# Optimization experiments

Hardware: AMD Instinct MI355X
Metric: run time of the kernel (lower is better)

## Reference

```python
import jax, jax.numpy as jnp
import numpy as np

P, M, DG, F, H, DH = 2000, 150, 2000, 256, 4, 64
N1, N2 = P + M, P + DG          # adj1 nodes (patient+med), adj2 nodes (patient+diag)
E1, E2, EGP, EGM = 137600, 256000, 64000, 4800
GNN_LAYERS = 2
SA_HID = 128


def setup_inputs() -> dict:
    key = jax.random.key(0)
    ks = jax.random.split(key, 32)
    ri = lambda k, n, hi: jax.random.randint(k, (n,), 0, hi, dtype=jnp.int32)
    rn = lambda k, shape, scale: (jax.random.normal(k, shape, dtype=jnp.float32) * scale)
    inp = {
        'adj1_rows': ri(ks[0], E1, N1), 'adj1_cols': ri(ks[1], E1, N1),
        'adj1_vals': jax.random.uniform(ks[2], (E1,), dtype=jnp.float32),
        'adj2_rows': ri(ks[3], E2, N2), 'adj2_cols': ri(ks[4], E2, N2),
        'adj2_vals': jax.random.uniform(ks[5], (E2,), dtype=jnp.float32),
        'g0_src': ri(ks[6], EGP, P), 'g0_dst': ri(ks[7], EGP, P),
        'g1_src': ri(ks[8], EGP, P), 'g1_dst': ri(ks[9], EGP, P),
        'g2_src': ri(ks[10], EGM, M), 'g2_dst': ri(ks[11], EGM, M),
        'g3_src': ri(ks[12], EGM, M), 'g3_dst': ri(ks[13], EGM, M),
        'keepRate': 1,
        # learned parameters (xavier-ish scales)
        'pEmbed': rn(ks[14], (P, F), 0.05),
        'mEmbed': rn(ks[15], (M, F), 0.05),
        'dEmbed': rn(ks[16], (DG, F), 0.05),
        'gat_W': rn(ks[17], (4, F, H * DH), (2.0 / (F + H * DH)) ** 0.5),
        'gat_al': rn(ks[18], (4, H, DH), 0.1),
        'gat_ar': rn(ks[19], (4, H, DH), 0.1),
        'gat_b': jnp.zeros((4, H * DH), dtype=jnp.float32),
        'sa_W1': rn(ks[20], (H * DH, SA_HID), (2.0 / (H * DH + SA_HID)) ** 0.5),
        'sa_b1': jnp.zeros((SA_HID,), dtype=jnp.float32),
        'sa_W2': rn(ks[21], (SA_HID, 1), 0.1),
        'out_W': rn(ks[22], (2 * F, M), (2.0 / (2 * F + M)) ** 0.5),
        'out_b': jnp.zeros((M,), dtype=jnp.float32),
    }
    return inp


def _spmm(rows, cols, vals, x, n):
    # sparse adj @ x via gather + segment_sum
    return jax.ops.segment_sum(vals[:, None] * x[cols], rows, num_segments=n)


def _seg_softmax(e, seg, n):
    m = jax.ops.segment_max(e, seg, num_segments=n)          # [n, H]
    ex = jnp.exp(e - m[seg])
    s = jax.ops.segment_sum(ex, seg, num_segments=n)
    return ex / (s[seg] + 1e-9)


def _gat(h, W, al, ar, b, src, dst, n):
    # DGL GATConv, feat/attn dropout = 0, negative_slope = 0.2, activation = elu
    feat = (h @ W).reshape(n, H, DH)                          # [n, H, DH]
    el = (feat * al[None]).sum(-1)                            # [n, H]
    er = (feat * ar[None]).sum(-1)
    e = jax.nn.leaky_relu(el[src] + er[dst], negative_slope=0.2)  # [E, H]
    alpha = _seg_softmax(e, dst, n)                           # softmax over in-edges per dst
    out = jax.ops.segment_sum(alpha[:, :, None] * feat[src], dst, num_segments=n)
    out = out + b.reshape(1, H, DH)
    return jax.nn.elu(out).reshape(n, H * DH)


def _sem_att(z, W1, b1, W2):
    # z: [N, K, F]; shared projection; beta over K meta-paths
    w = (jnp.tanh(z @ W1 + b1) @ W2).mean(0)                  # [K, 1]
    beta = jax.nn.softmax(w, axis=0)                          # [K, 1]
    return (beta[None] * z).sum(1)                            # [N, F]


def reference(adj1_rows, adj1_cols, adj1_vals, adj2_rows, adj2_cols, adj2_vals,
              g0_src, g0_dst, g1_src, g1_dst, g2_src, g2_dst, g3_src, g3_dst,
              keepRate, pEmbed, mEmbed, dEmbed, gat_W, gat_al, gat_ar, gat_b,
              sa_W1, sa_b1, sa_W2, out_W, out_b):
    embeds1 = jnp.concatenate([pEmbed, mEmbed], axis=0)       # [N1, F]
    embeds2 = jnp.concatenate([pEmbed, dEmbed], axis=0)       # [N2, F]
    lat1, lat2 = embeds1, embeds2
    acc1 = jnp.zeros_like(embeds1)
    acc2 = jnp.zeros_like(embeds2)
    for _ in range(GNN_LAYERS):
        lat1 = jax.nn.leaky_relu(_spmm(adj1_rows, adj1_cols, adj1_vals, lat1, N1), negative_slope=0.5)
        lat2 = jax.nn.leaky_relu(_spmm(adj2_rows, adj2_cols, adj2_vals, lat2, N2), negative_slope=0.5)
        acc1 = acc1 + lat1
        acc2 = acc2 + lat2
    p1, m_gcn = acc1[:P], acc1[P:]
    p2, d_gcn = acc2[:P], acc2[P:]

    e0 = _gat(p1, gat_W[0], gat_al[0], gat_ar[0], gat_b[0], g0_src, g0_dst, P)
    e1 = _gat(p2, gat_W[1], gat_al[1], gat_ar[1], gat_b[1], g1_src, g1_dst, P)
    e2 = _gat(m_gcn, gat_W[2], gat_al[2], gat_ar[2], gat_b[2], g2_src, g2_dst, M)
    e3 = _gat(m_gcn, gat_W[3], gat_al[3], gat_ar[3], gat_b[3], g3_src, g3_dst, M)

    patient = _sem_att(jnp.stack([e0, e1], axis=1), sa_W1, sa_b1, sa_W2)  # [P, F]
    med = _sem_att(jnp.stack([e2, e3], axis=1), sa_W1, sa_b1, sa_W2)      # [M, F]

    # broadcasted pairwise concat -> ReLU -> Linear -> sum over pairing axis
    pm = jnp.concatenate([
        jnp.broadcast_to(patient[:, None, :], (P, M, F)),
        jnp.broadcast_to(med[None, :, :], (P, M, F)),
    ], axis=-1).reshape(P * M, 2 * F)
    simi = (jax.nn.relu(pm) @ out_W + out_b).reshape(P, M, M)
    simi_pm = simi.sum(axis=1)                                # [P, M]
    return (simi_pm, d_gcn, med, m_gcn, patient)
```

## Files before the change

### kernel.cpp

```cpp
#include <hip/hip_runtime.h>
#include <cmath>
#include <cstdint>

constexpr int P  = 2000, M = 150, DG = 2000, F = 256, H = 4, DH = 64;
constexpr int N1 = P + M;
constexpr int N2 = P + DG;
constexpr int E1 = 137600, E2 = 256000, EGP = 64000, EGM = 4800;
constexpr int SA_HID = 128;

constexpr int HO1 = E1, HO2 = E1 + E2, HO3 = HO2 + EGP, HO4 = HO3 + EGP,
              HO5 = HO4 + EGM, HOE = HO5 + EGM;

constexpr int CAP_A = 160;
constexpr int CAP_G = 96;
constexpr int OVF_CAP = 4096;

__global__ __launch_bounds__(256) void k_build(
    const int* __restrict__ a1r, const int* __restrict__ a1c, const float* __restrict__ a1v,
    const int* __restrict__ a2r, const int* __restrict__ a2c, const float* __restrict__ a2v,
    const int* __restrict__ d0, const int* __restrict__ s0,
    const int* __restrict__ d1, const int* __restrict__ s1,
    const int* __restrict__ d2, const int* __restrict__ s2,
    const int* __restrict__ d3, const int* __restrict__ s3,
    int* cur1, uint2* ell1, int* cur2, uint2* ell2,
    int* cu0, unsigned* eg0, int* cu1, unsigned* eg1,
    int* cu2, unsigned* eg2, int* cu3, unsigned* eg3,
    int* __restrict__ ovf_n, int4* __restrict__ ovf) {
  int tid = blockIdx.x * 256 + threadIdx.x;
  int T = gridDim.x * 256;
  auto edge = [&](int i) {
    if (i >= HOE) return;
    if (i < HO1) {
      int r = a1r[i];
      int slot = atomicAdd(&cur1[r], 1);
      uint2 pl = {(unsigned)a1c[i], __float_as_uint(a1v[i])};
      if (slot < CAP_A) ell1[(size_t)r * CAP_A + slot] = pl;
      else { int o = atomicAdd(&ovf_n[0], 1); if (o < OVF_CAP) ovf[0 * OVF_CAP + o] = make_int4(r, (int)pl.x, (int)pl.y, 0); }
    } else if (i < HO2) {
      int j = i - HO1;
      int r = a2r[j];
      int slot = atomicAdd(&cur2[r], 1);
      uint2 pl = {(unsigned)a2c[j], __float_as_uint(a2v[j])};
      if (slot < CAP_A) ell2[(size_t)r * CAP_A + slot] = pl;
      else { int o = atomicAdd(&ovf_n[1], 1); if (o < OVF_CAP) ovf[1 * OVF_CAP + o] = make_int4(r, (int)pl.x, (int)pl.y, 0); }
    } else if (i < HO3) {
      int j = i - HO2; int r = d0[j];
      int slot = atomicAdd(&cu0[r], 1);
      if (slot < CAP_G) eg0[(size_t)r * CAP_G + slot] = (unsigned)s0[j];
      else { int o = atomicAdd(&ovf_n[2], 1); if (o < OVF_CAP) ovf[2 * OVF_CAP + o] = make_int4(r, s0[j], 0, 0); }
    } else if (i < HO4) {
      int j = i - HO3; int r = d1[j];
      int slot = atomicAdd(&cu1[r], 1);
      if (slot < CAP_G) eg1[(size_t)r * CAP_G + slot] = (unsigned)s1[j];
      else { int o = atomicAdd(&ovf_n[3], 1); if (o < OVF_CAP) ovf[3 * OVF_CAP + o] = make_int4(r, s1[j], 0, 0); }
    } else if (i < HO5) {
      int j = i - HO4; int r = d2[j];
      int slot = atomicAdd(&cu2[r], 1);
      if (slot < CAP_G) eg2[(size_t)r * CAP_G + slot] = (unsigned)s2[j];
      else { int o = atomicAdd(&ovf_n[4], 1); if (o < OVF_CAP) ovf[4 * OVF_CAP + o] = make_int4(r, s2[j], 0, 0); }
    } else {
      int j = i - HO5; int r = d3[j];
      int slot = atomicAdd(&cu3[r], 1);
      if (slot < CAP_G) eg3[(size_t)r * CAP_G + slot] = (unsigned)s3[j];
      else { int o = atomicAdd(&ovf_n[5], 1); if (o < OVF_CAP) ovf[5 * OVF_CAP + o] = make_int4(r, s3[j], 0, 0); }
    }
  };
  edge(tid);
  edge(tid + T);
  edge(tid + 2 * T);
  edge(tid + 3 * T);
}

template<int LAYER>
__global__ __launch_bounds__(256) void k_spmm(
    const int* __restrict__ cur1, const uint2* __restrict__ ell1,
    const int* __restrict__ cur2, const uint2* __restrict__ ell2,
    const int* __restrict__ ovf_n, const int4* __restrict__ ovf,
    const float* __restrict__ pE, const float* __restrict__ mE, const float* __restrict__ dE,
    float* __restrict__ lat1, float* __restrict__ lat2,
    float* __restrict__ acc1, float* __restrict__ acc2,
    float* __restrict__ out_mgcn, float* __restrict__ out_dgcn) {
  int gw = (blockIdx.x * 256 + threadIdx.x) >> 6;
  if (gw >= N1 + N2) return;
  int lane = threadIdx.x & 63;
  bool g2 = gw >= N1;
  int row = g2 ? gw - N1 : gw;
  const uint2* pe = (g2 ? ell2 : ell1) + (size_t)row * CAP_A;
  const float* latin = g2 ? lat2 : lat1;
  const float* tailE = g2 ? dE : mE;
  int deg = (g2 ? cur2 : cur1)[row];
  int dn = deg < CAP_A ? deg : CAP_A;
  int fo = lane << 2;
  float4 s = {0.f, 0.f, 0.f, 0.f};
  auto fetch = [&](int c) -> float4 {
    const float* b;
    if (LAYER == 1) b = (c < P) ? (pE + (size_t)c * F) : (tailE + (size_t)(c - P) * F);
    else            b = latin + (size_t)c * F;
    return *(const float4*)(b + fo);
  };
  int i = 0;
  for (; i + 4 <= dn; i += 4) {
    uint2 m0 = pe[i], m1 = pe[i + 1], m2 = pe[i + 2], m3 = pe[i + 3];
    float v0 = __uint_as_float(m0.y), v1 = __uint_as_float(m1.y),
          v2 = __uint_as_float(m2.y), v3 = __uint_as_float(m3.y);
    float4 a0 = fetch((int)m0.x), a1 = fetch((int)m1.x),
           a2 = fetch((int)m2.x), a3 = fetch((int)m3.x);
    s.x += v0 * a0.x + v1 * a1.x + v2 * a2.x + v3 * a3.x;
    s.y += v0 * a0.y + v1 * a1.y + v2 * a2.y + v3 * a3.y;
    s.z += v0 * a0.z + v1 * a1.z + v2 * a2.z + v3 * a3.z;
    s.w += v0 * a0.w + v1 * a1.w + v2 * a2.w + v3 * a3.w;
  }
  for (; i < dn; ++i) {
    uint2 m = pe[i];
    float v = __uint_as_float(m.y);
    float4 a = fetch((int)m.x);
    s.x += v * a.x; s.y += v * a.y; s.z += v * a.z; s.w += v * a.w;
  }
  {
    int gi = g2 ? 1 : 0;
    int on = ovf_n[gi];
    if (on > 0) {
      const int4* ol = ovf + gi * OVF_CAP;
      for (int k = 0; k < on; ++k) {
        int4 e = ol[k];
        if (e.x == row) {
          float v = __int_as_float(e.z);
          float4 a = fetch(e.y);
          s.x += v * a.x; s.y += v * a.y; s.z += v * a.z; s.w += v * a.w;
        }
      }
    }
  }
  float4 l;
  l.x = s.x > 0.f ? s.x : 0.5f * s.x;
  l.y = s.y > 0.f ? s.y : 0.5f * s.y;
  l.z = s.z > 0.f ? s.z : 0.5f * s.z;
  l.w = s.w > 0.f ? s.w : 0.5f * s.w;
  if (LAYER == 1) {
    *(float4*)((g2 ? lat2 : lat1) + (size_t)row * F + fo) = l;
  } else {
    float4 b = *(const float4*)(latin + (size_t)row * F + fo);
    float4 a = {b.x + l.x, b.y + l.y, b.z + l.z, b.w + l.w};
    *(float4*)((g2 ? acc2 : acc1) + (size_t)row * F + fo) = a;
    if (row >= P)
      *(float4*)((g2 ? out_dgcn : out_mgcn) + (size_t)(row - P) * F + fo) = a;
  }
}

constexpr int FR  = 4;
constexpr int NB0 = (P + FR - 1) / FR;
constexpr int NB2 = (M + FR - 1) / FR;
constexpr int FEAT_BLOCKS = 2 * NB0 + 2 * NB2;

__global__ __launch_bounds__(256) void k_gat_feat_all(
    const float* __restrict__ acc1, const float* __restrict__ acc2,
    const float* __restrict__ gat_W, const float* __restrict__ gat_al,
    const float* __restrict__ gat_ar,
    float* __restrict__ f0, float* __restrict__ f1,
    float* __restrict__ f2, float* __restrict__ f3,
    float* __restrict__ el, float* __restrict__ er) {
  int b = blockIdx.x;
  int g, rb, n; const float* h; float* fout;
  if (b < NB0)            { g = 0; rb = b;              n = P; h = acc1; fout = f0; }
  else if (b < 2 * NB0)   { g = 1; rb = b - NB0;        n = P; h = acc2; fout = f1; }
  else if (b < 2*NB0+NB2) { g = 2; rb = b - 2 * NB0;    n = M; h = acc1 + (size_t)P * F; fout = f2; }
  else                    { g = 3; rb = b - 2*NB0 - NB2; n = M; h = acc1 + (size_t)P * F; fout = f3; }
  int elo = (g == 0) ? 0 : (g == 1) ? P * H : (g == 2) ? 2 * P * H : (2 * P + M) * H;
  const float* W = gat_W + (size_t)g * F * F;
  __shared__ float hs[FR][F];
  int t = threadIdx.x;
  int r0 = rb * FR;
  {
    int r = t >> 6, ln = t & 63;
    int row = r0 + r;
    float4 v = {0.f, 0.f, 0.f, 0.f};
    if (row < n) v = *(const float4*)(h + (size_t)row * F + (ln << 2));
    *(float4*)&hs[r][ln << 2] = v;
  }
  __syncthreads();
  float acc[FR] = {0.f, 0.f, 0.f, 0.f};
  for (int k = 0; k < F; k += 4) {
    float w0 = W[(size_t)k * F + t],       w1 = W[(size_t)(k + 1) * F + t],
          w2 = W[(size_t)(k + 2) * F + t], w3 = W[(size_t)(k + 3) * F + t];
#pragma unroll
    for (int r = 0; r < FR; ++r) {
      float4 h4 = *(const float4*)&hs[r][k];
      acc[r] += h4.x * w0 + h4.y * w1 + h4.z * w2 + h4.w * w3;
    }
  }
  int head = t >> 6, d = t & 63;
  float av = gat_al[g * H * DH + head * DH + d];
  float rv = gat_ar[g * H * DH + head * DH + d];
#pragma unroll
  for (int r = 0; r < FR; ++r) {
    int row = r0 + r;
    if (row < n) {
      fout[(size_t)row * F + t] = acc[r];
      float cl = acc[r] * av, cr = acc[r] * rv;
      for (int o = 32; o > 0; o >>= 1) {
        cl += __shfl_down(cl, o, 64);
        cr += __shfl_down(cr, o, 64);
      }
      if (d == 0) { el[elo + row * H + head] = cl; er[elo + row * H + head] = cr; }
    }
  }
}

__global__ __launch_bounds__(256) void k_gat_agg_all(
    const int* __restrict__ cu0, const unsigned* __restrict__ eg0,
    const int* __restrict__ cu1, const unsigned* __restrict__ eg1,
    const int* __restrict__ cu2, const unsigned* __restrict__ eg2,
    const int* __restrict__ cu3, const unsigned* __restrict__ eg3,
    const int* __restrict__ ovf_n, const int4* __restrict__ ovf,
    const float* __restrict__ el, const float* __restrict__ er,
    const float* __restrict__ f0, const float* __restrict__ f1,
    const float* __restrict__ f2, const float* __restrict__ f3,
    const float* __restrict__ gat_b,
    float* __restrict__ e0, float* __restrict__ e1,
    float* __restrict__ e2, float* __restrict__ e3) {
  int gw = (blockIdx.x * 256 + threadIdx.x) >> 6;
  if (gw >= 2 * P + 2 * M) return;
  int lane = threadIdx.x & 63;
  int g, row; const int* cu; const unsigned* eg; const float* feat; float* out; int elo;
  if (gw < P)            { g = 0; row = gw;             cu = cu0; eg = eg0; feat = f0; out = e0; elo = 0; }
  else if (gw < 2 * P)   { g = 1; row = gw - P;         cu = cu1; eg = eg1; feat = f1; out = e1; elo = P * H; }
  else if (gw < 2*P + M) { g = 2; row = gw - 2 * P;     cu = cu2; eg = eg2; feat = f2; out = e2; elo = 2 * P * H; }
  else                   { g = 3; row = gw - 2 * P - M; cu = cu3; eg = eg3; feat = f3; out = e3; elo = (2 * P + M) * H; }
  int head = lane >> 4;
  int fo = lane << 2;
  const float* elb = el + elo;
  float erv = er[elo + row * H + head];
  int deg = cu[row];
  int dn = deg < CAP_G ? deg : CAP_G;
  const unsigned* ps = eg + (size_t)row * CAP_G;
  int on = ovf_n[2 + g];
  const int4* ol = ovf + (2 + g) * OVF_CAP;
  float mx = -3.4e38f;
  int i = 0;
  for (; i + 4 <= dn; i += 4) {
    int s0 = (int)ps[i], s1 = (int)ps[i + 1], s2 = (int)ps[i + 2], s3 = (int)ps[i + 3];
    float a = elb[s0 * H + head] + erv, b = elb[s1 * H + head] + erv,
          c = elb[s2 * H + head] + erv, d = elb[s3 * H + head] + erv;
    a = a > 0.f ? a : 0.2f * a; b = b > 0.f ? b : 0.2f * b;
    c = c > 0.f ? c : 0.2f * c; d = d > 0.f ? d : 0.2f * d;
    mx = fmaxf(mx, fmaxf(fmaxf(a, b), fmaxf(c, d)));
  }
  for (; i < dn; ++i) {
    float a = elb[(int)ps[i] * H + head] + erv;
    a = a > 0.f ? a : 0.2f * a;
    mx = fmaxf(mx, a);
  }
  if (on > 0) {
    for (int k = 0; k < on; ++k) {
      int4 e = ol[k];
      if (e.x == row) {
        float a = elb[e.y * H + head] + erv;
        a = a > 0.f ? a : 0.2f * a;
        mx = fmaxf(mx, a);
      }
    }
  }
  float ssum = 0.f;
  float4 acc = {0.f, 0.f, 0.f, 0.f};
  i = 0;
  for (; i + 2 <= dn; i += 2) {
    int s0 = (int)ps[i], s1 = (int)ps[i + 1];
    float a = elb[s0 * H + head] + erv; a = a > 0.f ? a : 0.2f * a;
    float b = elb[s1 * H + head] + erv; b = b > 0.f ? b : 0.2f * b;
    float x0 = expf(a - mx), x1 = expf(b - mx);
    float4 q0 = *(const float4*)(feat + (size_t)s0 * F + fo);
    float4 q1 = *(const float4*)(feat + (size_t)s1 * F + fo);
    ssum += x0 + x1;
    acc.x += x0 * q0.x + x1 * q1.x;
    acc.y += x0 * q0.y + x1 * q1.y;
    acc.z += x0 * q0.z + x1 * q1.z;
    acc.w += x0 * q0.w + x1 * q1.w;
  }
  for (; i < dn; ++i) {
    int s0 = (int)ps[i];
    float a = elb[s0 * H + head] + erv; a = a > 0.f ? a : 0.2f * a;
    float x0 = expf(a - mx);
    float4 q0 = *(const float4*)(feat + (size_t)s0 * F + fo);
    ssum += x0;
    acc.x += x0 * q0.x; acc.y += x0 * q0.y; acc.z += x0 * q0.z; acc.w += x0 * q0.w;
  }
  if (on > 0) {
    for (int k = 0; k < on; ++k) {
      int4 e = ol[k];
      if (e.x == row) {
        float a = elb[e.y * H + head] + erv; a = a > 0.f ? a : 0.2f * a;
        float x0 = expf(a - mx);
        float4 q0 = *(const float4*)(feat + (size_t)e.y * F + fo);
        ssum += x0;
        acc.x += x0 * q0.x; acc.y += x0 * q0.y; acc.z += x0 * q0.z; acc.w += x0 * q0.w;
      }
    }
  }
  float inv = 1.f / (ssum + 1e-9f);
  const float* bb = gat_b + g * F + fo;
  float4 v = {acc.x * inv + bb[0], acc.y * inv + bb[1],
              acc.z * inv + bb[2], acc.w * inv + bb[3]};
  v.x = v.x > 0.f ? v.x : expm1f(v.x);
  v.y = v.y > 0.f ? v.y : expm1f(v.y);
  v.z = v.z > 0.f ? v.z : expm1f(v.z);
  v.w = v.w > 0.f ? v.w : expm1f(v.w);
  *(float4*)(out + (size_t)row * F + fo) = v;
}

constexpr int SR  = 8;
constexpr int SB0 = (P + SR - 1) / SR;
constexpr int SB2 = (M + SR - 1) / SR;
constexpr int SEM_BLOCKS = 2 * SB0 + 2 * SB2;

__global__ __launch_bounds__(128) void k_sem_w_all(
    const float* __restrict__ e0, const float* __restrict__ e1,
    const float* __restrict__ e2, const float* __restrict__ e3,
    const float* __restrict__ W1, const float* __restrict__ b1,
    const float* __restrict__ W2, float* __restrict__ w) {
  int b = blockIdx.x;
  int zid, rb, n; const float* z;
  if (b < SB0)            { zid = 0; rb = b;             n = P; z = e0; }
  else if (b < 2 * SB0)   { zid = 1; rb = b - SB0;       n = P; z = e1; }
  else if (b < 2*SB0+SB2) { zid = 2; rb = b - 2 * SB0;   n = M; z = e2; }
  else                    { zid = 3; rb = b - 2*SB0-SB2; n = M; z = e3; }
  __shared__ float zs[SR][F];
  int t = threadIdx.x;
  int r0 = rb * SR;
  for (int q = t; q < SR * 64; q += 128) {
    int r = q >> 6, ln = q & 63;
    int row = r0 + r;
    float4 v = {0.f, 0.f, 0.f, 0.f};
    if (row < n) v = *(const float4*)(z + (size_t)row * F + (ln << 2));
    *(float4*)&zs[r][ln << 2] = v;
  }
  __syncthreads();
  float hid[SR];
#pragma unroll
  for (int r = 0; r < SR; ++r) hid[r] = b1[t];
  for (int k = 0; k < F; k += 4) {
    float w0 = W1[(size_t)k * SA_HID + t],       w1 = W1[(size_t)(k + 1) * SA_HID + t],
          w2 = W1[(size_t)(k + 2) * SA_HID + t], w3 = W1[(size_t)(k + 3) * SA_HID + t];
#pragma unroll
    for (int r = 0; r < SR; ++r) {
      float4 z4 = *(const float4*)&zs[r][k];
      hid[r] += z4.x * w0 + z4.y * w1 + z4.z * w2 + z4.w * w3;
    }
  }
  float w2v = W2[t];
  float local = 0.f;
  for (int r = 0; r < SR; ++r) {
    int row = r0 + r;
    if (row < n) local += tanhf(hid[r]) * w2v;
  }
  for (int o = 32; o > 0; o >>= 1) local += __shfl_down(local, o, 64);
  __shared__ float pp[2];
  if ((t & 63) == 0) pp[t >> 6] = local;
  __syncthreads();
  if (t == 0) atomicAdd(&w[zid], pp[0] + pp[1]);
}

__global__ void k_sem_comb_all(const float* __restrict__ e0, const float* __restrict__ e1,
                               const float* __restrict__ e2, const float* __restrict__ e3,
                               const float* __restrict__ w,
                               float* __restrict__ out_pat, float* __restrict__ out_med) {
  constexpr int Q0 = P * F / 4;
  constexpr int QE = Q0 + M * F / 4;
  int i = blockIdx.x * 256 + threadIdx.x;
  if (i >= QE) return;
  const float4 *z0, *z1; float* out; float inv_n; const float* wp; int j;
  if (i < Q0) { z0 = (const float4*)e0; z1 = (const float4*)e1; out = out_pat; inv_n = 1.f / P; wp = w;     j = i; }
  else        { z0 = (const float4*)e2; z1 = (const float4*)e3; out = out_med; inv_n = 1.f / M; wp = w + 2; j = i - Q0; }
  float m0 = wp[0] * inv_n, m1 = wp[1] * inv_n;
  float mxv = fmaxf(m0, m1);
  float a0 = expf(m0 - mxv), a1 = expf(m1 - mxv);
  float s = 1.f / (a0 + a1);
  a0 *= s; a1 *= s;
  float4 u0 = z0[j], u1 = z1[j];
  float4 r = {a0 * u0.x + a1 * u1.x, a0 * u0.y + a1 * u1.y,
              a0 * u0.z + a1 * u1.z, a0 * u0.w + a1 * u1.w};
  ((float4*)out)[j] = r;
}

__global__ void k_cvec(const float* __restrict__ med, const float* __restrict__ outW,
                       const float* __restrict__ outb, float* __restrict__ c) {
  __shared__ float sv[F];
  int t = threadIdx.x;
  float a = 0.f;
  for (int m = 0; m < M; ++m) { float v = med[(size_t)m * F + t]; a += v > 0.f ? v : 0.f; }
  sv[t] = a;
  __syncthreads();
  if (t < M) {
    float cc = (float)M * outb[t];
    for (int f = 0; f < F; ++f) cc += sv[f] * outW[(size_t)(F + f) * M + t];
    c[t] = cc;
  }
}

constexpr int FIN_R = 8;
__global__ __launch_bounds__(256) void k_final(const float* __restrict__ pat,
                                               const float* __restrict__ outW,
                                               const float* __restrict__ c,
                                               float* __restrict__ simi) {
  __shared__ float psh[FIN_R][F];
  int t = threadIdx.x;
  int r0 = blockIdx.x * FIN_R;
  for (int q = t; q < FIN_R * 64; q += 256) {
    int r = q >> 6, ln = q & 63;
    float4 v = *(const float4*)(pat + (size_t)(r0 + r) * F + (ln << 2));
    v.x = v.x > 0.f ? v.x : 0.f; v.y = v.y > 0.f ? v.y : 0.f;
    v.z = v.z > 0.f ? v.z : 0.f; v.w = v.w > 0.f ? v.w : 0.f;
    *(float4*)&psh[r][ln << 2] = v;
  }
  __syncthreads();
  if (t < M) {
    float acc[FIN_R];
#pragma unroll
    for (int r = 0; r < FIN_R; ++r) acc[r] = 0.f;
    for (int f = 0; f < F; f += 4) {
      float w0 = outW[(size_t)f * M + t],       w1 = outW[(size_t)(f + 1) * M + t],
            w2 = outW[(size_t)(f + 2) * M + t], w3 = outW[(size_t)(f + 3) * M + t];
#pragma unroll
      for (int r = 0; r < FIN_R; ++r) {
        float4 p4 = *(const float4*)&psh[r][f];
        acc[r] += p4.x * w0 + p4.y * w1 + p4.z * w2 + p4.w * w3;
      }
    }
    float cv = c[t];
    for (int r = 0; r < FIN_R; ++r)
      simi[(size_t)(r0 + r) * M + t] = (float)M * acc[r] + cv;
  }
}

extern "C" void kernel_launch(void* const* d_in, const int* in_sizes, int n_in,
                              void* d_out, int out_size, void* d_ws, size_t ws_size,
                              hipStream_t stream) {
  const int*   adj1_rows = (const int*)d_in[0];
  const int*   adj1_cols = (const int*)d_in[1];
  const float* adj1_vals = (const float*)d_in[2];
  const int*   adj2_rows = (const int*)d_in[3];
  const int*   adj2_cols = (const int*)d_in[4];
  const float* adj2_vals = (const float*)d_in[5];
  const int*   g0_src = (const int*)d_in[6];
  const int*   g0_dst = (const int*)d_in[7];
  const int*   g1_src = (const int*)d_in[8];
  const int*   g1_dst = (const int*)d_in[9];
  const int*   g2_src = (const int*)d_in[10];
  const int*   g2_dst = (const int*)d_in[11];
  const int*   g3_src = (const int*)d_in[12];
  const int*   g3_dst = (const int*)d_in[13];
  const float* pE     = (const float*)d_in[15];
  const float* mE     = (const float*)d_in[16];
  const float* dE     = (const float*)d_in[17];
  const float* gat_W  = (const float*)d_in[18];
  const float* gat_al = (const float*)d_in[19];
  const float* gat_ar = (const float*)d_in[20];
  const float* gat_b  = (const float*)d_in[21];
  const float* sa_W1  = (const float*)d_in[22];
  const float* sa_b1  = (const float*)d_in[23];
  const float* sa_W2  = (const float*)d_in[24];
  const float* out_W  = (const float*)d_in[25];
  const float* out_b  = (const float*)d_in[26];

  int* ip = (int*)d_ws;
  int* cur1 = ip; ip += N1;
  int* cur2 = ip; ip += N2;
  int* cu0  = ip; ip += P;
  int* cu1  = ip; ip += P;
  int* cu2  = ip; ip += M;
  int* cu3  = ip; ip += M;
  int* ovf_n = ip; ip += 6;
  float* wbuf = (float*)ip; ip += 4;
  size_t memset_bytes = (size_t)((char*)ip - (char*)d_ws);

  uintptr_t up = ((uintptr_t)ip + 15) & ~(uintptr_t)15;
  int4* ovf = (int4*)up;
  uint2* ell1 = (uint2*)(ovf + 6 * OVF_CAP);
  uint2* ell2 = ell1 + (size_t)N1 * CAP_A;
  unsigned* eg0 = (unsigned*)(ell2 + (size_t)N2 * CAP_A);
  unsigned* eg1 = eg0 + (size_t)P * CAP_G;
  unsigned* eg2 = eg1 + (size_t)P * CAP_G;
  unsigned* eg3 = eg2 + (size_t)M * CAP_G;
  float* fp = (float*)(eg3 + (size_t)M * CAP_G);
  float* lat1 = fp; fp += (size_t)N1 * F;
  float* lat2 = fp; fp += (size_t)N2 * F;
  float* acc1 = fp; fp += (size_t)N1 * F;
  float* acc2 = fp; fp += (size_t)N2 * F;
  float* f0   = fp; fp += (size_t)P * F;
  float* f1   = fp; fp += (size_t)P * F;
  float* f2   = fp; fp += (size_t)M * F;
  float* f3   = fp; fp += (size_t)M * F;
  float* el   = fp; fp += (size_t)(2 * P + 2 * M) * H;
  float* er   = fp; fp += (size_t)(2 * P + 2 * M) * H;
  float* e0b  = fp; fp += (size_t)P * F;
  float* e1b  = fp; fp += (size_t)P * F;
  float* e2b  = fp; fp += (size_t)M * F;
  float* e3b  = fp; fp += (size_t)M * F;
  float* cbuf = fp; fp += 256;

  float* out_simi = (float*)d_out;
  float* out_dgcn = out_simi + (size_t)P * M;
  float* out_med  = out_dgcn + (size_t)DG * F;
  float* out_mgcn = out_med  + (size_t)M * F;
  float* out_pat  = out_mgcn + (size_t)M * F;

  hipMemsetAsync(d_ws, 0, memset_bytes, stream);

  int eb = ((HOE + 3) / 4 + 255) / 256;
  k_build<<<eb, 256, 0, stream>>>(adj1_rows, adj1_cols, adj1_vals,
                                  adj2_rows, adj2_cols, adj2_vals,
                                  g0_dst, g0_src, g1_dst, g1_src,
                                  g2_dst, g2_src, g3_dst, g3_src,
                                  cur1, ell1, cur2, ell2,
                                  cu0, eg0, cu1, eg1, cu2, eg2, cu3, eg3,
                                  ovf_n, ovf);

  int sb = ((N1 + N2) * 64 + 255) / 256;
  k_spmm<1><<<sb, 256, 0, stream>>>(cur1, ell1, cur2, ell2, ovf_n, ovf, pE, mE, dE,
                                    lat1, lat2, acc1, acc2, out_mgcn, out_dgcn);
  k_spmm<2><<<sb, 256, 0, stream>>>(cur1, ell1, cur2, ell2, ovf_n, ovf, pE, mE, dE,
                                    lat1, lat2, acc1, acc2, out_mgcn, out_dgcn);

  k_gat_feat_all<<<FEAT_BLOCKS, 256, 0, stream>>>(acc1, acc2, gat_W, gat_al, gat_ar,
                                                  f0, f1, f2, f3, el, er);
  int ab = ((2 * P + 2 * M) * 64 + 255) / 256;
  k_gat_agg_all<<<ab, 256, 0, stream>>>(cu0, eg0, cu1, eg1, cu2, eg2, cu3, eg3,
                                        ovf_n, ovf, el, er, f0, f1, f2, f3, gat_b,
                                        e0b, e1b, e2b, e3b);

  k_sem_w_all<<<SEM_BLOCKS, 128, 0, stream>>>(e0b, e1b, e2b, e3b, sa_W1, sa_b1, sa_W2, wbuf);
  int cb = ((P * F + M * F) / 4 + 255) / 256;
  k_sem_comb_all<<<cb, 256, 0, stream>>>(e0b, e1b, e2b, e3b, wbuf, out_pat, out_med);

  k_cvec<<<1, 256, 0, stream>>>(out_med, out_W, out_b, cbuf);
  k_final<<<P / FIN_R, 256, 0, stream>>>(out_pat, out_W, cbuf, out_simi);
}
```

Measured before the change: 323.4 us.

## Fuse semantic combine into final and cvec kernels, unroll build and spmm

Folds the semantic-attention combine step into the final kernel for patients and into a new single-block med kernel that also computes the c vector. This drops one kernel launch and one write/read round trip of the combined embeddings. It also batches the index loads ahead of the atomics in the edge build, adds an 8-way unrolled gather loop in the SpMM, and doubles the rows per block in the GAT feature transform. The single-block med kernel serialises a small amount of work, and the larger unrolls raise register pressure.

```diff
diff --git a/kernel.cpp b/kernel.cpp
--- a/kernel.cpp
+++ b/kernel.cpp
@@ -28,47 +28,45 @@
     int* __restrict__ ovf_n, int4* __restrict__ ovf) {
   int tid = blockIdx.x * 256 + threadIdx.x;
   int T = gridDim.x * 256;
-  auto edge = [&](int i) {
-    if (i >= HOE) return;
-    if (i < HO1) {
-      int r = a1r[i];
-      int slot = atomicAdd(&cur1[r], 1);
-      uint2 pl = {(unsigned)a1c[i], __float_as_uint(a1v[i])};
-      if (slot < CAP_A) ell1[(size_t)r * CAP_A + slot] = pl;
-      else { int o = atomicAdd(&ovf_n[0], 1); if (o < OVF_CAP) ovf[0 * OVF_CAP + o] = make_int4(r, (int)pl.x, (int)pl.y, 0); }
-    } else if (i < HO2) {
-      int j = i - HO1;
-      int r = a2r[j];
-      int slot = atomicAdd(&cur2[r], 1);
-      uint2 pl = {(unsigned)a2c[j], __float_as_uint(a2v[j])};
-      if (slot < CAP_A) ell2[(size_t)r * CAP_A + slot] = pl;
-      else { int o = atomicAdd(&ovf_n[1], 1); if (o < OVF_CAP) ovf[1 * OVF_CAP + o] = make_int4(r, (int)pl.x, (int)pl.y, 0); }
-    } else if (i < HO3) {
-      int j = i - HO2; int r = d0[j];
-      int slot = atomicAdd(&cu0[r], 1);
-      if (slot < CAP_G) eg0[(size_t)r * CAP_G + slot] = (unsigned)s0[j];
-      else { int o = atomicAdd(&ovf_n[2], 1); if (o < OVF_CAP) ovf[2 * OVF_CAP + o] = make_int4(r, s0[j], 0, 0); }
-    } else if (i < HO4) {
-      int j = i - HO3; int r = d1[j];
-      int slot = atomicAdd(&cu1[r], 1);
-      if (slot < CAP_G) eg1[(size_t)r * CAP_G + slot] = (unsigned)s1[j];
-      else { int o = atomicAdd(&ovf_n[3], 1); if (o < OVF_CAP) ovf[3 * OVF_CAP + o] = make_int4(r, s1[j], 0, 0); }
-    } else if (i < HO5) {
-      int j = i - HO4; int r = d2[j];
-      int slot = atomicAdd(&cu2[r], 1);
-      if (slot < CAP_G) eg2[(size_t)r * CAP_G + slot] = (unsigned)s2[j];
-      else { int o = atomicAdd(&ovf_n[4], 1); if (o < OVF_CAP) ovf[4 * OVF_CAP + o] = make_int4(r, s2[j], 0, 0); }
-    } else {
-      int j = i - HO5; int r = d3[j];
-      int slot = atomicAdd(&cu3[r], 1);
-      if (slot < CAP_G) eg3[(size_t)r * CAP_G + slot] = (unsigned)s3[j];
-      else { int o = atomicAdd(&ovf_n[5], 1); if (o < OVF_CAP) ovf[5 * OVF_CAP + o] = make_int4(r, s3[j], 0, 0); }
-    }
-  };
-  edge(tid);
-  edge(tid + T);
-  edge(tid + 2 * T);
-  edge(tid + 3 * T);
+  int seg[4], row[4]; unsigned p0[4], p1[4];
+#pragma unroll
+  for (int u = 0; u < 4; ++u) {
+    int i = tid + u * T;
+    seg[u] = -1;
+    if (i < HOE) {
+      if (i < HO1)      { seg[u] = 0; row[u] = a1r[i]; p0[u] = (unsigned)a1c[i]; p1[u] = __float_as_uint(a1v[i]); }
+      else if (i < HO2) { int j = i - HO1; seg[u] = 1; row[u] = a2r[j]; p0[u] = (unsigned)a2c[j]; p1[u] = __float_as_uint(a2v[j]); }
+      else if (i < HO3) { int j = i - HO2; seg[u] = 2; row[u] = d0[j]; p0[u] = (unsigned)s0[j]; }
+      else if (i < HO4) { int j = i - HO3; seg[u] = 3; row[u] = d1[j]; p0[u] = (unsigned)s1[j]; }
+      else if (i < HO5) { int j = i - HO4; seg[u] = 4; row[u] = d2[j]; p0[u] = (unsigned)s2[j]; }
+      else              { int j = i - HO5; seg[u] = 5; row[u] = d3[j]; p0[u] = (unsigned)s3[j]; }
+    }
+  }
+#pragma unroll
+  for (int u = 0; u < 4; ++u) {
+    int r = row[u];
+    switch (seg[u]) {
+      case 0: { int slot = atomicAdd(&cur1[r], 1);
+        if (slot < CAP_A) ell1[(size_t)r * CAP_A + slot] = make_uint2(p0[u], p1[u]);
+        else { int o = atomicAdd(&ovf_n[0], 1); if (o < OVF_CAP) ovf[0 * OVF_CAP + o] = make_int4(r, (int)p0[u], (int)p1[u], 0); } } break;
+      case 1: { int slot = atomicAdd(&cur2[r], 1);
+        if (slot < CAP_A) ell2[(size_t)r * CAP_A + slot] = make_uint2(p0[u], p1[u]);
+        else { int o = atomicAdd(&ovf_n[1], 1); if (o < OVF_CAP) ovf[1 * OVF_CAP + o] = make_int4(r, (int)p0[u], (int)p1[u], 0); } } break;
+      case 2: { int slot = atomicAdd(&cu0[r], 1);
+        if (slot < CAP_G) eg0[(size_t)r * CAP_G + slot] = p0[u];
+        else { int o = atomicAdd(&ovf_n[2], 1); if (o < OVF_CAP) ovf[2 * OVF_CAP + o] = make_int4(r, (int)p0[u], 0, 0); } } break;
+      case 3: { int slot = atomicAdd(&cu1[r], 1);
+        if (slot < CAP_G) eg1[(size_t)r * CAP_G + slot] = p0[u];
+        else { int o = atomicAdd(&ovf_n[3], 1); if (o < OVF_CAP) ovf[3 * OVF_CAP + o] = make_int4(r, (int)p0[u], 0, 0); } } break;
+      case 4: { int slot = atomicAdd(&cu2[r], 1);
+        if (slot < CAP_G) eg2[(size_t)r * CAP_G + slot] = p0[u];
+        else { int o = atomicAdd(&ovf_n[4], 1); if (o < OVF_CAP) ovf[4 * OVF_CAP + o] = make_int4(r, (int)p0[u], 0, 0); } } break;
+      case 5: { int slot = atomicAdd(&cu3[r], 1);
+        if (slot < CAP_G) eg3[(size_t)r * CAP_G + slot] = p0[u];
+        else { int o = atomicAdd(&ovf_n[5], 1); if (o < OVF_CAP) ovf[5 * OVF_CAP + o] = make_int4(r, (int)p0[u], 0, 0); } } break;
+      default: break;
+    }
+  }
 }
 
 template<int LAYER>
@@ -99,6 +97,18 @@
     return *(const float4*)(b + fo);
   };
   int i = 0;
+  for (; i + 8 <= dn; i += 8) {
+    uint2 m[8]; float4 a[8];
+#pragma unroll
+    for (int u = 0; u < 8; ++u) m[u] = pe[i + u];
+#pragma unroll
+    for (int u = 0; u < 8; ++u) a[u] = fetch((int)m[u].x);
+#pragma unroll
+    for (int u = 0; u < 8; ++u) {
+      float v = __uint_as_float(m[u].y);
+      s.x += v * a[u].x; s.y += v * a[u].y; s.z += v * a[u].z; s.w += v * a[u].w;
+    }
+  }
   for (; i + 4 <= dn; i += 4) {
     uint2 m0 = pe[i], m1 = pe[i + 1], m2 = pe[i + 2], m3 = pe[i + 3];
     float v0 = __uint_as_float(m0.y), v1 = __uint_as_float(m1.y),
@@ -147,7 +157,7 @@
   }
 }
 
-constexpr int FR  = 4;
+constexpr int FR  = 8;
 constexpr int NB0 = (P + FR - 1) / FR;
 constexpr int NB2 = (M + FR - 1) / FR;
 constexpr int FEAT_BLOCKS = 2 * NB0 + 2 * NB2;
@@ -170,15 +180,17 @@
   __shared__ float hs[FR][F];
   int t = threadIdx.x;
   int r0 = rb * FR;
-  {
-    int r = t >> 6, ln = t & 63;
+  for (int q = t; q < FR * 64; q += 256) {
+    int r = q >> 6, ln = q & 63;
     int row = r0 + r;
     float4 v = {0.f, 0.f, 0.f, 0.f};
     if (row < n) v = *(const float4*)(h + (size_t)row * F + (ln << 2));
     *(float4*)&hs[r][ln << 2] = v;
   }
   __syncthreads();
-  float acc[FR] = {0.f, 0.f, 0.f, 0.f};
+  float acc[FR];
+#pragma unroll
+  for (int r = 0; r < FR; ++r) acc[r] = 0.f;
   for (int k = 0; k < F; k += 4) {
     float w0 = W[(size_t)k * F + t],       w1 = W[(size_t)(k + 1) * F + t],
           w2 = W[(size_t)(k + 2) * F + t], w3 = W[(size_t)(k + 3) * F + t];
@@ -359,54 +371,73 @@
   if (t == 0) atomicAdd(&w[zid], pp[0] + pp[1]);
 }
 
-__global__ void k_sem_comb_all(const float* __restrict__ e0, const float* __restrict__ e1,
-                               const float* __restrict__ e2, const float* __restrict__ e3,
-                               const float* __restrict__ w,
-                               float* __restrict__ out_pat, float* __restrict__ out_med) {
-  constexpr int Q0 = P * F / 4;
-  constexpr int QE = Q0 + M * F / 4;
-  int i = blockIdx.x * 256 + threadIdx.x;
-  if (i >= QE) return;
-  const float4 *z0, *z1; float* out; float inv_n; const float* wp; int j;
-  if (i < Q0) { z0 = (const float4*)e0; z1 = (const float4*)e1; out = out_pat; inv_n = 1.f / P; wp = w;     j = i; }
-  else        { z0 = (const float4*)e2; z1 = (const float4*)e3; out = out_med; inv_n = 1.f / M; wp = w + 2; j = i - Q0; }
-  float m0 = wp[0] * inv_n, m1 = wp[1] * inv_n;
+__global__ __launch_bounds__(256) void k_med_cvec(
+    const float* __restrict__ e2, const float* __restrict__ e3,
+    const float* __restrict__ w, const float* __restrict__ outW,
+    const float* __restrict__ outb,
+    float* __restrict__ out_med, float* __restrict__ cbuf) {
+  int t = threadIdx.x;
+  float m0 = w[2] * (1.f / M), m1 = w[3] * (1.f / M);
   float mxv = fmaxf(m0, m1);
   float a0 = expf(m0 - mxv), a1 = expf(m1 - mxv);
-  float s = 1.f / (a0 + a1);
-  a0 *= s; a1 *= s;
-  float4 u0 = z0[j], u1 = z1[j];
-  float4 r = {a0 * u0.x + a1 * u1.x, a0 * u0.y + a1 * u1.y,
-              a0 * u0.z + a1 * u1.z, a0 * u0.w + a1 * u1.w};
-  ((float4*)out)[j] = r;
-}
-
-__global__ void k_cvec(const float* __restrict__ med, const float* __restrict__ outW,
-                       const float* __restrict__ outb, float* __restrict__ c) {
+  float sc = 1.f / (a0 + a1);
+  a0 *= sc; a1 *= sc;
+  float4 rs = {0.f, 0.f, 0.f, 0.f};
+  for (int j = t; j < M * F / 4; j += 256) {
+    float4 u0 = ((const float4*)e2)[j], u1 = ((const float4*)e3)[j];
+    float4 r = {a0 * u0.x + a1 * u1.x, a0 * u0.y + a1 * u1.y,
+                a0 * u0.z + a1 * u1.z, a0 * u0.w + a1 * u1.w};
+    ((float4*)out_med)[j] = r;
+    rs.x += r.x > 0.f ? r.x : 0.f;
+    rs.y += r.y > 0.f ? r.y : 0.f;
+    rs.z += r.z > 0.f ? r.z : 0.f;
+    rs.w += r.w > 0.f ? r.w : 0.f;
+  }
+  __shared__ float4 sv4[4][64];
+  sv4[t >> 6][t & 63] = rs;
+  __syncthreads();
   __shared__ float sv[F];
-  int t = threadIdx.x;
-  float a = 0.f;
-  for (int m = 0; m < M; ++m) { float v = med[(size_t)m * F + t]; a += v > 0.f ? v : 0.f; }
-  sv[t] = a;
+  if (t < 64) {
+    float4 a = sv4[0][t], b = sv4[1][t], c = sv4[2][t], d = sv4[3][t];
+    sv[t * 4 + 0] = a.x + b.x + c.x + d.x;
+    sv[t * 4 + 1] = a.y + b.y + c.y + d.y;
+    sv[t * 4 + 2] = a.z + b.z + c.z + d.z;
+    sv[t * 4 + 3] = a.w + b.w + c.w + d.w;
+  }
   __syncthreads();
   if (t < M) {
     float cc = (float)M * outb[t];
-    for (int f = 0; f < F; ++f) cc += sv[f] * outW[(size_t)(F + f) * M + t];
-    c[t] = cc;
+    for (int f = 0; f < F; f += 4) {
+      cc += sv[f]     * outW[(size_t)(F + f) * M + t]
+          + sv[f + 1] * outW[(size_t)(F + f + 1) * M + t]
+          + sv[f + 2] * outW[(size_t)(F + f + 2) * M + t]
+          + sv[f + 3] * outW[(size_t)(F + f + 3) * M + t];
+    }
+    cbuf[t] = cc;
   }
 }
 
 constexpr int FIN_R = 8;
-__global__ __launch_bounds__(256) void k_final(const float* __restrict__ pat,
-                                               const float* __restrict__ outW,
-                                               const float* __restrict__ c,
-                                               float* __restrict__ simi) {
+__global__ __launch_bounds__(256) void k_final(
+    const float* __restrict__ e0, const float* __restrict__ e1,
+    const float* __restrict__ w, const float* __restrict__ outW,
+    const float* __restrict__ c,
+    float* __restrict__ out_pat, float* __restrict__ simi) {
+  float m0 = w[0] * (1.f / P), m1 = w[1] * (1.f / P);
+  float mxv = fmaxf(m0, m1);
+  float a0 = expf(m0 - mxv), a1 = expf(m1 - mxv);
+  float sc = 1.f / (a0 + a1);
+  a0 *= sc; a1 *= sc;
   __shared__ float psh[FIN_R][F];
   int t = threadIdx.x;
   int r0 = blockIdx.x * FIN_R;
   for (int q = t; q < FIN_R * 64; q += 256) {
     int r = q >> 6, ln = q & 63;
-    float4 v = *(const float4*)(pat + (size_t)(r0 + r) * F + (ln << 2));
+    size_t off = (size_t)(r0 + r) * F + (ln << 2);
+    float4 u0 = *(const float4*)(e0 + off), u1 = *(const float4*)(e1 + off);
+    float4 v = {a0 * u0.x + a1 * u1.x, a0 * u0.y + a1 * u1.y,
+                a0 * u0.z + a1 * u1.z, a0 * u0.w + a1 * u1.w};
+    *(float4*)(out_pat + off) = v;
     v.x = v.x > 0.f ? v.x : 0.f; v.y = v.y > 0.f ? v.y : 0.f;
     v.z = v.z > 0.f ? v.z : 0.f; v.w = v.w > 0.f ? v.w : 0.f;
     *(float4*)&psh[r][ln << 2] = v;
@@ -528,9 +559,8 @@
                                         e0b, e1b, e2b, e3b);
 
   k_sem_w_all<<<SEM_BLOCKS, 128, 0, stream>>>(e0b, e1b, e2b, e3b, sa_W1, sa_b1, sa_W2, wbuf);
-  int cb = ((P * F + M * F) / 4 + 255) / 256;
-  k_sem_comb_all<<<cb, 256, 0, stream>>>(e0b, e1b, e2b, e3b, wbuf, out_pat, out_med);
-
-  k_cvec<<<1, 256, 0, stream>>>(out_med, out_W, out_b, cbuf);
-  k_final<<<P / FIN_R, 256, 0, stream>>>(out_pat, out_W, cbuf, out_simi);
-}
+
+  k_med_cvec<<<1, 256, 0, stream>>>(e2b, e3b, wbuf, out_W, out_b, out_med, cbuf);
+
+  k_final<<<P / FIN_R, 256, 0, stream>>>(e0b, e1b, wbuf, out_W, cbuf, out_pat, out_simi);
+}
```

Result: no change. 325.0 us (+0.5%).
